# Kernel tuning notes

Measured on AMD Instinct MI355X. Metric: run time of the kernel, lower is better.

## Reference

```python
import jax, jax.numpy as jnp
import numpy as np

EPS = 1e-5
NUM_GRAPHS = 512


def _glorot(key, shape):
    lim = float(np.sqrt(6.0 / (shape[0] + shape[1])))
    return jax.random.uniform(key, shape, jnp.float32, -lim, lim)


def setup_inputs() -> dict:
    key = jax.random.key(0)
    ks = jax.random.split(key, 20)
    N, E, F0 = 50000, 800000, 64
    x = jax.random.normal(ks[0], (N, F0), jnp.float32)
    edge_index = jax.random.randint(ks[1], (2, E), 0, N, jnp.int64)
    batch = jnp.sort(jax.random.randint(ks[2], (N,), 0, NUM_GRAPHS, jnp.int64))
    dims = [(F0, 128), (128, 64), (64, 32)]
    p = {}
    for i, (di, do) in enumerate(dims, start=1):
        p[f"W{i}l"] = _glorot(ks[3 * i], (di, do))
        p[f"b{i}"] = jnp.zeros((do,), jnp.float32)
        p[f"W{i}r"] = _glorot(ks[3 * i + 1], (di, do))
        p[f"g{i}"] = jnp.ones((do,), jnp.float32)
        p[f"be{i}"] = jnp.zeros((do,), jnp.float32)
    p["Wf1"] = _glorot(ks[13], (32, 128)); p["bf1"] = jnp.zeros((128,), jnp.float32)
    p["Wf2"] = _glorot(ks[14], (128, 64)); p["bf2"] = jnp.zeros((64,), jnp.float32)
    p["Wf3"] = _glorot(ks[15], (64, 2)); p["bf3"] = jnp.zeros((2,), jnp.float32)
    return {"x": x, "edge_index": edge_index, "batch": batch, **p}


def _sage(x, src, dst, Wl, bl, Wr, n):
    # mean-aggregate neighbor features (gather from src, scatter-mean to dst)
    agg = jax.ops.segment_sum(x[src], dst, num_segments=n)
    cnt = jax.ops.segment_sum(jnp.ones((src.shape[0],), x.dtype), dst, num_segments=n)
    mean = agg / jnp.maximum(cnt, 1.0)[:, None]
    return mean @ Wl + bl + x @ Wr


def _bn(x, g, b):
    mu = jnp.mean(x, axis=0)
    var = jnp.mean((x - mu) ** 2, axis=0)  # biased var, torch training mode
    return (x - mu) * jax.lax.rsqrt(var + EPS) * g + b


def reference(x, edge_index, batch,
              W1l, b1, W1r, g1, be1,
              W2l, b2, W2r, g2, be2,
              W3l, b3, W3r, g3, be3,
              Wf1, bf1, Wf2, bf2, Wf3, bf3):
    n = x.shape[0]
    src, dst = edge_index[0], edge_index[1]
    h = _bn(jax.nn.relu(_sage(x, src, dst, W1l, b1, W1r, n)), g1, be1)
    h = _bn(jax.nn.relu(_sage(h, src, dst, W2l, b2, W2r, n)), g2, be2)
    h = _bn(jax.nn.relu(_sage(h, src, dst, W3l, b3, W3r, n)), g3, be3)
    pooled = jax.ops.segment_sum(h, batch, num_segments=NUM_GRAPHS)  # [G, 32]
    cr = jax.nn.relu(pooled @ Wf1 + bf1)  # dropout = identity (eval)
    cr = jax.nn.relu(cr @ Wf2 + bf2)
    cr = cr @ Wf3 + bf3
    return cr.reshape(-1, 2)
```

## Files before the change

### kernel.cpp

```cpp
#include <hip/hip_runtime.h>
#include <hip/hip_bf16.h>

#define EPSBN 1e-5f
#define NGRAPH 512
#define SCAN_NB 128

typedef __attribute__((ext_vector_type(8))) short bf16x8;
typedef __attribute__((ext_vector_type(4))) float f32x4;

__device__ inline short f2bf(float f) {
    unsigned u = __builtin_bit_cast(unsigned, f);
    u += 0x7fffu + ((u >> 16) & 1u);
    return (short)(u >> 16);
}
__device__ inline float bf2f(short s) {
    unsigned u = ((unsigned)(unsigned short)s) << 16;
    return __builtin_bit_cast(float, u);
}
__device__ inline int xcd_id() {
    int x;
    asm volatile("s_getreg_b32 %0, hwreg(HW_REG_XCC_ID, 0, 4)" : "=s"(x));
    return x & 7;
}

__global__ void __launch_bounds__(256) k_hist8(
    const int* __restrict__ dst, int* __restrict__ hist8, int E, int Npad)
{
    int* h = hist8 + xcd_id() * Npad;
    const int stride = gridDim.x * 256;
    for (int e = blockIdx.x * 256 + threadIdx.x; e < E; e += stride)
        atomicAdd(&h[dst[e]], 1);
}

__global__ void __launch_bounds__(256) k_scan1(
    const int* __restrict__ hist8, int* __restrict__ blocksum, int N, int Npad)
{
    __shared__ int red[256];
    const int C = (N + SCAN_NB - 1) / SCAN_NB;
    const int b = blockIdx.x, t = threadIdx.x;
    const int lo = b * C, hi = min(lo + C, N);
    int s = 0;
    for (int i = lo + t; i < hi; i += 256) {
        int v = 0;
        #pragma unroll
        for (int c = 0; c < 8; c++) v += hist8[c * Npad + i];
        s += v;
    }
    red[t] = s;
    __syncthreads();
    for (int off = 128; off; off >>= 1) {
        if (t < off) red[t] += red[t + off];
        __syncthreads();
    }
    if (t == 0) blocksum[b] = red[0];
}

__global__ void __launch_bounds__(256) k_scan3(
    const int* __restrict__ hist8, const int* __restrict__ blocksum,
    int* __restrict__ row_off, int* __restrict__ cursor, int N, int Npad)
{
    __shared__ int red[256];
    __shared__ int boff_s;
    const int C = (N + SCAN_NB - 1) / SCAN_NB;
    const int b = blockIdx.x, t = threadIdx.x;
    const int lo = b * C, hi = min(lo + C, N);
    if (t == 0) {
        int acc = 0;
        for (int i = 0; i < b; i++) acc += blocksum[i];
        boff_s = acc;
        if (b == SCAN_NB - 1) {
            int tot = acc;
            for (int i = b; i < SCAN_NB; i++) tot += blocksum[i];
            row_off[N] = tot;
        }
    }
    const int TC = (C + 255) / 256;
    const int s0 = lo + t * TC;
    const int s1 = min(s0 + TC, hi);
    auto hsum = [&](int i) {
        int v = 0;
        #pragma unroll
        for (int c = 0; c < 8; c++) v += hist8[c * Npad + i];
        return v;
    };
    int s = 0;
    for (int i = s0; i < s1; i++) s += hsum(i);
    red[t] = s;
    __syncthreads();
    for (int off = 1; off < 256; off <<= 1) {
        int u = (t >= off) ? red[t - off] : 0;
        __syncthreads();
        red[t] += u;
        __syncthreads();
    }
    int run = boff_s + red[t] - s;
    for (int i = s0; i < s1; i++) {
        row_off[i] = run;
        cursor[i] = run;
        run += hsum(i);
    }
}

__global__ void __launch_bounds__(256) k_scatter(
    const int* __restrict__ src, const int* __restrict__ dst,
    int* __restrict__ cursor, int* __restrict__ csr, int E)
{
    for (int e = blockIdx.x * 256 + threadIdx.x; e < E; e += gridDim.x * 256) {
        int d = dst[e];
        int p = atomicAdd(&cursor[d], 1);
        csr[p] = src[e];
    }
}

__device__ inline int lbound(const int* __restrict__ a, int n, int v) {
    int lo = 0, hi = n;
    while (lo < hi) {
        int mid = (lo + hi) >> 1;
        if (a[mid] < v) lo = mid + 1; else hi = mid;
    }
    return lo;
}
__global__ void __launch_bounds__(256) k_gcnt_bs(
    const int* __restrict__ batch, float* __restrict__ gcnt, int N)
{
    int g = blockIdx.x * 256 + threadIdx.x;
    if (g < NGRAPH)
        gcnt[g] = (float)(lbound(batch, N, g + 1) - lbound(batch, N, g));
}

template <int F>
__global__ void __launch_bounds__(256) k_gatherb(
    const short* __restrict__ feat, const int* __restrict__ row_off,
    const int* __restrict__ csr, short* __restrict__ aggb, int N)
{
    constexpr int LPR = F / 8;
    constexpr int RPB = 256 / LPR;
    const int lane = threadIdx.x % LPR;
    const int rloc = threadIdx.x / LPR;
    const short* fbase = feat + lane * 8;
    for (int row = blockIdx.x * RPB + rloc; row < N; row += gridDim.x * RPB) {
        const int s0 = row_off[row];
        const int s1 = row_off[row + 1];
        float acc0[8], acc1[8], acc2[8], acc3[8];
        #pragma unroll
        for (int i = 0; i < 8; i++) {
            acc0[i] = 0.f; acc1[i] = 0.f; acc2[i] = 0.f; acc3[i] = 0.f;
        }
        int p = s0;
        for (; p + 3 < s1; p += 4) {
            int sA = csr[p], sB = csr[p + 1], sC = csr[p + 2], sD = csr[p + 3];
            bf16x8 va = *(const bf16x8*)&fbase[(long long)sA * F];
            bf16x8 vb = *(const bf16x8*)&fbase[(long long)sB * F];
            bf16x8 vc = *(const bf16x8*)&fbase[(long long)sC * F];
            bf16x8 vd = *(const bf16x8*)&fbase[(long long)sD * F];
            #pragma unroll
            for (int i = 0; i < 8; i++) {
                acc0[i] += bf2f(va[i]);
                acc1[i] += bf2f(vb[i]);
                acc2[i] += bf2f(vc[i]);
                acc3[i] += bf2f(vd[i]);
            }
        }
        for (; p < s1; p++) {
            int sA = csr[p];
            bf16x8 va = *(const bf16x8*)&fbase[(long long)sA * F];
            #pragma unroll
            for (int i = 0; i < 8; i++) acc0[i] += bf2f(va[i]);
        }
        short o[8];
        #pragma unroll
        for (int i = 0; i < 8; i++)
            o[i] = f2bf((acc0[i] + acc1[i]) + (acc2[i] + acc3[i]));
        *(bf16x8*)&aggb[(long long)row * F + lane * 8] = *(bf16x8*)o;
    }
}

__global__ void __launch_bounds__(256) k_cvt(
    const float* __restrict__ in, short* __restrict__ out, long long n4)
{
    long long i = (long long)blockIdx.x * 256 + threadIdx.x;
    if (i >= n4) return;
    float4 v = *(const float4*)&in[i * 4];
    short4 o = make_short4(f2bf(v.x), f2bf(v.y), f2bf(v.z), f2bf(v.w));
    *(short4*)&out[i * 4] = o;
}

template <int K, int F, bool AFF>
__global__ void __launch_bounds__(64) k_wprep2(
    const float* __restrict__ Wl, const float* __restrict__ Wr,
    const float* __restrict__ a, const float* __restrict__ c,
    const float* __restrict__ bias,
    short* __restrict__ Wlt, short* __restrict__ Wrt,
    float* __restrict__ cvl, float* __restrict__ cvr)
{
    int j = blockIdx.x * 64 + threadIdx.x;
    const bool second = j >= F;
    const int jj = second ? j - F : j;
    if (jj >= F || j >= 2 * F) return;
    const float* W = second ? Wr : Wl;
    short* Wt = second ? Wrt : Wlt;
    float cv = (second && bias) ? bias[jj] : 0.f;
    for (int k = 0; k < K; k++) {
        float w = W[k * F + jj];
        float aa = 1.f;
        if constexpr (AFF) {
            aa = a[k];
            cv += c[k] * w;
        }
        Wt[jj * K + k] = f2bf(aa * w);
    }
    if (second) cvr[jj] = cv; else cvl[jj] = cv;
}

template <int K, int FOUT, bool DUAL, bool HASBASE, bool FINAL, bool OUTBF16,
          bool POOL>
__global__ void __launch_bounds__(256) k_mgemm(
    const short* __restrict__ A, const short* __restrict__ A2,
    const short* __restrict__ Wt, const short* __restrict__ Wt2,
    const float* __restrict__ cvec, const short* __restrict__ base,
    const int* __restrict__ row_off, void* outv,
    float* __restrict__ s_out, float* __restrict__ q_out,
    const int* __restrict__ batchp, float* __restrict__ praw8, int N)
{
    constexpr int KS = K / 32;
    constexpr int NCT = FOUT / 16;
    const int lane = threadIdx.x & 63;
    const int wid = threadIdx.x >> 6;
    const int g = lane >> 4;
    const int mi = lane & 15;
    const int RT = (N + 15) >> 4;
    const int nw = gridDim.x * 4;
    float* outf = (float*)outv;
    short* outb = (short*)outv;
    float* pr = nullptr;
    if constexpr (POOL) pr = praw8 + (size_t)xcd_id() * NGRAPH * 32;

    float st_s[FINAL ? NCT : 1];
    float st_q[FINAL ? NCT : 1];
    if constexpr (FINAL) {
        #pragma unroll
        for (int ct = 0; ct < NCT; ct++) { st_s[ct] = 0.f; st_q[ct] = 0.f; }
    }

    for (int rt = blockIdx.x * 4 + wid; rt < RT; rt += nw) {
        const int m0 = rt * 16;
        int arow = m0 + mi;
        if (arow >= N) arow = N - 1;

        bf16x8 af[KS];
        bf16x8 af2[DUAL ? KS : 1];
        const short* ap = A + (long long)arow * K;
        #pragma unroll
        for (int s = 0; s < KS; s++)
            af[s] = *(const bf16x8*)(ap + s * 32 + g * 8);
        if constexpr (DUAL) {
            const short* ap2 = A2 + (long long)arow * K;
            #pragma unroll
            for (int s = 0; s < KS; s++)
                af2[s] = *(const bf16x8*)(ap2 + s * 32 + g * 8);
        }

        float invc[4];
        if constexpr (DUAL || HASBASE) {
            #pragma unroll
            for (int r = 0; r < 4; r++) {
                int row = m0 + 4 * g + r;
                int cnt = 1;
                if (row < N) cnt = max(row_off[row + 1] - row_off[row], 1);
                invc[r] = 1.f / (float)cnt;
            }
        }
        int bidx[4];
        if constexpr (POOL) {
            #pragma unroll
            for (int r = 0; r < 4; r++) {
                int row = m0 + 4 * g + r;
                bidx[r] = (row < N) ? batchp[row] : -1;
            }
        }

        #pragma unroll
        for (int ct = 0; ct < NCT; ct++) {
            f32x4 acc = {0.f, 0.f, 0.f, 0.f};
            f32x4 acc2 = {0.f, 0.f, 0.f, 0.f};
            const short* bp = Wt + (long long)(ct * 16 + mi) * K;
            #pragma unroll
            for (int s = 0; s < KS; s++) {
                bf16x8 bf = *(const bf16x8*)(bp + s * 32 + g * 8);
                acc = __builtin_amdgcn_mfma_f32_16x16x32_bf16(af[s], bf, acc, 0, 0, 0);
                if constexpr (DUAL) {
                    bf16x8 bf2 = *(const bf16x8*)(Wt2 + (long long)(ct * 16 + mi) * K + s * 32 + g * 8);
                    acc2 = __builtin_amdgcn_mfma_f32_16x16x32_bf16(af2[s], bf2, acc2, 0, 0, 0);
                }
            }
            float cv = cvec[ct * 16 + mi];
            float sl = 0.f, ql = 0.f;
            #pragma unroll
            for (int r = 0; r < 4; r++) {
                int row = m0 + 4 * g + r;
                if (row < N) {
                    float v = acc[r] + cv;
                    if constexpr (DUAL) v = fmaf(invc[r], acc2[r], v);
                    if constexpr (HASBASE)
                        v = fmaf(invc[r], bf2f(base[(long long)row * FOUT + ct * 16 + mi]), v);
                    if constexpr (FINAL) v = fmaxf(v, 0.f);
                    if constexpr (POOL) {
                        atomicAdd(&pr[bidx[r] * FOUT + ct * 16 + mi], v);
                    } else if constexpr (OUTBF16) {
                        outb[(long long)row * FOUT + ct * 16 + mi] = f2bf(v);
                    } else {
                        outf[(long long)row * FOUT + ct * 16 + mi] = v;
                    }
                    if constexpr (FINAL) { sl += v; ql += v * v; }
                }
            }
            if constexpr (FINAL) {
                sl += __shfl_xor(sl, 16, 64);
                sl += __shfl_xor(sl, 32, 64);
                ql += __shfl_xor(ql, 16, 64);
                ql += __shfl_xor(ql, 32, 64);
                st_s[ct] += sl;
                st_q[ct] += ql;
            }
        }
    }

    if constexpr (FINAL) {
        __shared__ float redS[4][NCT][16];
        __shared__ float redQ[4][NCT][16];
        if (lane < 16) {
            #pragma unroll
            for (int ct = 0; ct < NCT; ct++) {
                redS[wid][ct][lane] = st_s[ct];
                redQ[wid][ct][lane] = st_q[ct];
            }
        }
        __syncthreads();
        if (wid == 0 && lane < 16) {
            #pragma unroll
            for (int ct = 0; ct < NCT; ct++) {
                float s = redS[0][ct][lane] + redS[1][ct][lane] +
                          redS[2][ct][lane] + redS[3][ct][lane];
                float q = redQ[0][ct][lane] + redQ[1][ct][lane] +
                          redQ[2][ct][lane] + redQ[3][ct][lane];
                atomicAdd(&s_out[ct * 16 + lane], s);
                atomicAdd(&q_out[ct * 16 + lane], q);
            }
        }
    }
}

__global__ void k_finalize(const float* __restrict__ s, const float* __restrict__ q,
                           const float* __restrict__ g, const float* __restrict__ be,
                           float* __restrict__ a, float* __restrict__ c,
                           int F, float invN)
{
    int j = threadIdx.x;
    if (j < F) {
        float mu = s[j] * invN;
        float var = q[j] * invN - mu * mu;
        float aj = g[j] / sqrtf(var + EPSBN);
        a[j] = aj;
        c[j] = be[j] - mu * aj;
    }
}

__global__ void __launch_bounds__(128) k_mlp(
    const float* __restrict__ praw8, const float* __restrict__ a3,
    const float* __restrict__ c3, const float* __restrict__ gcnt,
    const float* __restrict__ Wf1, const float* __restrict__ bf1,
    const float* __restrict__ Wf2, const float* __restrict__ bf2,
    const float* __restrict__ Wf3, const float* __restrict__ bf3,
    float* __restrict__ out)
{
    __shared__ float p[32], h1[128], h2[64];
    int g = blockIdx.x, t = threadIdx.x;
    if (t < 32) {
        float s = 0.f;
        #pragma unroll
        for (int c = 0; c < 8; c++)
            s += praw8[(size_t)c * NGRAPH * 32 + g * 32 + t];
        p[t] = a3[t] * s + gcnt[g] * c3[t];
    }
    __syncthreads();
    {
        float acc = bf1[t];
        #pragma unroll
        for (int k = 0; k < 32; k++) acc += p[k] * Wf1[k * 128 + t];
        h1[t] = fmaxf(acc, 0.f);
    }
    __syncthreads();
    if (t < 64) {
        float acc = bf2[t];
        #pragma unroll
        for (int k = 0; k < 128; k++) acc += h1[k] * Wf2[k * 64 + t];
        h2[t] = fmaxf(acc, 0.f);
    }
    __syncthreads();
    if (t < 2) {
        float acc = bf3[t];
        #pragma unroll
        for (int k = 0; k < 64; k++) acc += h2[k] * Wf3[k * 2 + t];
        out[g * 2 + t] = acc;
    }
}

extern "C" void kernel_launch(void* const* d_in, const int* in_sizes, int n_in,
                              void* d_out, int out_size, void* d_ws, size_t ws_size,
                              hipStream_t stream)
{
    const float* x     = (const float*)d_in[0];
    const int*   ei    = (const int*)d_in[1];
    const int*   batch = (const int*)d_in[2];
    const float* W1l = (const float*)d_in[3];
    const float* b1  = (const float*)d_in[4];
    const float* W1r = (const float*)d_in[5];
    const float* g1  = (const float*)d_in[6];
    const float* be1 = (const float*)d_in[7];
    const float* W2l = (const float*)d_in[8];
    const float* b2  = (const float*)d_in[9];
    const float* W2r = (const float*)d_in[10];
    const float* g2  = (const float*)d_in[11];
    const float* be2 = (const float*)d_in[12];
    const float* W3l = (const float*)d_in[13];
    const float* b3  = (const float*)d_in[14];
    const float* W3r = (const float*)d_in[15];
    const float* g3  = (const float*)d_in[16];
    const float* be3 = (const float*)d_in[17];
    const float* Wf1 = (const float*)d_in[18];
    const float* bf1 = (const float*)d_in[19];
    const float* Wf2 = (const float*)d_in[20];
    const float* bf2 = (const float*)d_in[21];
    const float* Wf3 = (const float*)d_in[22];
    const float* bf3 = (const float*)d_in[23];

    const int N = in_sizes[0] / 64;
    const int E = in_sizes[1] / 2;
    const int Npad = (N + 255) & ~255;
    const int* src = ei;
    const int* dst = ei + E;

    char* ws = (char*)d_ws;
    size_t off = 0;
    auto alloc = [&](size_t bytes) {
        size_t o = off;
        off += (bytes + 511) & ~(size_t)511;
        return o;
    };
    const size_t o_rowoff = alloc((size_t)(N + 1) * 4);
    const size_t o_cursor = alloc((size_t)N * 4);
    const size_t o_bsum   = alloc(SCAN_NB * 4);
    const size_t o_csr    = alloc((size_t)E * 4);
    const size_t o_zoneB  = alloc((size_t)N * 128);
    const size_t o_zoneC  = alloc((size_t)N * 128);
    const size_t o_zoneD  = alloc((size_t)N * 256);
    const size_t o_zoneE  = alloc((size_t)N * 128);
    const size_t o_aff    = alloc(448 * 4);
    const size_t o_cvec   = alloc(512 * 4);
    const size_t o_wt     = alloc((8192 * 4 + 2048 * 2) * 2);
    const size_t o_gcnt   = alloc((size_t)NGRAPH * 4);
    const size_t o_zero0  = off;
    const size_t o_hist8  = alloc((size_t)Npad * 8 * 4);
    const size_t o_stats  = alloc(448 * 4);
    const size_t o_praw8  = alloc((size_t)NGRAPH * 32 * 4 * 8);
    const size_t zero_len = off - o_zero0;
    (void)ws_size;

    int* row_off = (int*)(ws + o_rowoff);
    int* hist8   = (int*)(ws + o_hist8);
    int* cursor  = (int*)(ws + o_cursor);
    int* bsum    = (int*)(ws + o_bsum);
    int* csr     = (int*)(ws + o_csr);
    short* xb   = (short*)(ws + o_zoneB);
    short* y2b  = (short*)(ws + o_zoneB);
    short* aggb = (short*)(ws + o_zoneC);
    short* t2b  = (short*)(ws + o_zoneC);
    short* t1b  = (short*)(ws + o_zoneD);
    short* y3b  = (short*)(ws + o_zoneD);
    short* m2b  = (short*)(ws + o_zoneE);
    short* m3b  = (short*)(ws + o_zoneE);
    float* praw8 = (float*)(ws + o_praw8);
    float* gcnt  = (float*)(ws + o_gcnt);
    float* s1 = (float*)(ws + o_stats);
    float* q1 = s1 + 128;
    float* s2 = q1 + 128;
    float* q2 = s2 + 64;
    float* s3 = q2 + 64;
    float* q3 = s3 + 32;
    float* a1 = (float*)(ws + o_aff);
    float* c1 = a1 + 128;
    float* a2 = c1 + 128;
    float* c2 = a2 + 64;
    float* a3 = c2 + 64;
    float* c3 = a3 + 32;
    float* cv1l = (float*)(ws + o_cvec);
    float* cv1r = cv1l + 128;
    float* cv2l = cv1r + 128;
    float* cv2r = cv2l + 64;
    float* cv3l = cv2r + 64;
    float* cv3r = cv3l + 32;
    short* W1l_t = (short*)(ws + o_wt);
    short* W1r_t = W1l_t + 8192;
    short* W2l_t = W1r_t + 8192;
    short* W2r_t = W2l_t + 8192;
    short* W3l_t = W2r_t + 8192;
    short* W3r_t = W3l_t + 2048;

    const float invN = 1.0f / (float)N;
    const int MG = 512;

    hipMemsetAsync(ws + o_zero0, 0, zero_len, stream);

    k_hist8<<<2048, 256, 0, stream>>>(dst, hist8, E, Npad);
    k_scan1<<<SCAN_NB, 256, 0, stream>>>(hist8, bsum, N, Npad);
    k_scan3<<<SCAN_NB, 256, 0, stream>>>(hist8, bsum, row_off, cursor, N, Npad);
    k_scatter<<<2048, 256, 0, stream>>>(src, dst, cursor, csr, E);
    k_gcnt_bs<<<2, 256, 0, stream>>>(batch, gcnt, N);

    k_cvt<<<(int)(((long long)N * 16 + 255) / 256), 256, 0, stream>>>(
        x, xb, (long long)N * 16);
    k_wprep2<64, 128, false><<<4, 64, 0, stream>>>(
        W1l, W1r, nullptr, nullptr, b1, W1l_t, W1r_t, cv1l, cv1r);

    k_gatherb<64><<<(N + 31) / 32, 256, 0, stream>>>(
        xb, row_off, csr, aggb, N);
    k_mgemm<64, 128, true, false, true, true, false><<<MG, 256, 0, stream>>>(
        xb, aggb, W1r_t, W1l_t, cv1r, nullptr, row_off, t1b, s1, q1,
        nullptr, nullptr, N);
    k_finalize<<<1, 128, 0, stream>>>(s1, q1, g1, be1, a1, c1, 128, invN);

    k_wprep2<128, 64, true><<<2, 64, 0, stream>>>(
        W2l, W2r, a1, c1, b2, W2l_t, W2r_t, cv2l, cv2r);
    k_mgemm<128, 64, false, false, false, true, false><<<MG, 256, 0, stream>>>(
        t1b, nullptr, W2l_t, nullptr, cv2l, nullptr, row_off, y2b,
        nullptr, nullptr, nullptr, nullptr, N);
    k_gatherb<64><<<(N + 31) / 32, 256, 0, stream>>>(
        y2b, row_off, csr, m2b, N);
    k_mgemm<128, 64, false, true, true, true, false><<<MG, 256, 0, stream>>>(
        t1b, nullptr, W2r_t, nullptr, cv2r, m2b, row_off, t2b, s2, q2,
        nullptr, nullptr, N);
    k_finalize<<<1, 64, 0, stream>>>(s2, q2, g2, be2, a2, c2, 64, invN);

    k_wprep2<64, 32, true><<<1, 64, 0, stream>>>(
        W3l, W3r, a2, c2, b3, W3l_t, W3r_t, cv3l, cv3r);
    k_mgemm<64, 32, false, false, false, true, false><<<MG, 256, 0, stream>>>(
        t2b, nullptr, W3l_t, nullptr, cv3l, nullptr, row_off, y3b,
        nullptr, nullptr, nullptr, nullptr, N);
    k_gatherb<32><<<(N + 63) / 64, 256, 0, stream>>>(
        y3b, row_off, csr, m3b, N);
    k_mgemm<64, 32, false, true, true, false, true><<<MG, 256, 0, stream>>>(
        t2b, nullptr, W3r_t, nullptr, cv3r, m3b, row_off, nullptr, s3, q3,
        batch, praw8, N);
    k_finalize<<<1, 32, 0, stream>>>(s3, q3, g3, be3, a3, c3, 32, invN);

    k_mlp<<<NGRAPH, 128, 0, stream>>>(praw8, a3, c3, gcnt,
                                      Wf1, bf1, Wf2, bf2, Wf3, bf3,
                                      (float*)d_out);
}
```

Baseline: 300.3 us.

## Fuse small prep kernels, resize GEMM grid, trim gather accumulators

Merges the fp32-to-bf16 conversion of x into the histogram kernel and folds the per-graph count binary search into the first scan kernel, removing two launches. Scatter now writes CSR entries with nontemporal stores. The gather kernel gets an occupancy hint and uses two accumulator sets instead of four to lower register pressure. The GEMM grid is sized from N (one block per four 16-row tiles) instead of a fixed 512 blocks. Changing the grid assumes k_mgemm's internal row mapping matches the new block count, and the gather summation order changes slightly.

```diff
diff --git a/kernel.cpp b/kernel.cpp
--- a/kernel.cpp
+++ b/kernel.cpp
@@ -23,21 +23,42 @@
     return x & 7;
 }
 
-__global__ void __launch_bounds__(256) k_hist8(
-    const int* __restrict__ dst, int* __restrict__ hist8, int E, int Npad)
+__global__ void __launch_bounds__(256) k_hist_cvt(
+    const int* __restrict__ dst, int* __restrict__ hist8,
+    const float* __restrict__ x, short* __restrict__ xb,
+    int E, int Npad, long long n4)
 {
     int* h = hist8 + xcd_id() * Npad;
     const int stride = gridDim.x * 256;
     for (int e = blockIdx.x * 256 + threadIdx.x; e < E; e += stride)
         atomicAdd(&h[dst[e]], 1);
+    for (long long i = blockIdx.x * 256 + threadIdx.x; i < n4; i += stride) {
+        float4 v = *(const float4*)&x[i * 4];
+        short4 o = make_short4(f2bf(v.x), f2bf(v.y), f2bf(v.z), f2bf(v.w));
+        *(short4*)&xb[i * 4] = o;
+    }
+}
+
+__device__ inline int lbound(const int* __restrict__ a, int n, int v) {
+    int lo = 0, hi = n;
+    while (lo < hi) {
+        int mid = (lo + hi) >> 1;
+        if (a[mid] < v) lo = mid + 1; else hi = mid;
+    }
+    return lo;
 }
 
 __global__ void __launch_bounds__(256) k_scan1(
-    const int* __restrict__ hist8, int* __restrict__ blocksum, int N, int Npad)
+    const int* __restrict__ hist8, int* __restrict__ blocksum,
+    const int* __restrict__ batch, float* __restrict__ gcnt,
+    int N, int Npad)
 {
     __shared__ int red[256];
     const int C = (N + SCAN_NB - 1) / SCAN_NB;
     const int b = blockIdx.x, t = threadIdx.x;
+    const int g = b * 256 + t;
+    if (g < NGRAPH)
+        gcnt[g] = (float)(lbound(batch, N, g + 1) - lbound(batch, N, g));
     const int lo = b * C, hi = min(lo + C, N);
     int s = 0;
     for (int i = lo + t; i < hi; i += 256) {
@@ -108,28 +129,12 @@
     for (int e = blockIdx.x * 256 + threadIdx.x; e < E; e += gridDim.x * 256) {
         int d = dst[e];
         int p = atomicAdd(&cursor[d], 1);
-        csr[p] = src[e];
-    }
-}
-
-__device__ inline int lbound(const int* __restrict__ a, int n, int v) {
-    int lo = 0, hi = n;
-    while (lo < hi) {
-        int mid = (lo + hi) >> 1;
-        if (a[mid] < v) lo = mid + 1; else hi = mid;
-    }
-    return lo;
-}
-__global__ void __launch_bounds__(256) k_gcnt_bs(
-    const int* __restrict__ batch, float* __restrict__ gcnt, int N)
-{
-    int g = blockIdx.x * 256 + threadIdx.x;
-    if (g < NGRAPH)
-        gcnt[g] = (float)(lbound(batch, N, g + 1) - lbound(batch, N, g));
+        __builtin_nontemporal_store(src[e], &csr[p]);
+    }
 }
 
 template <int F>
-__global__ void __launch_bounds__(256) k_gatherb(
+__global__ void __launch_bounds__(256, 8) k_gatherb(
     const short* __restrict__ feat, const int* __restrict__ row_off,
     const int* __restrict__ csr, short* __restrict__ aggb, int N)
 {
@@ -141,11 +146,9 @@
     for (int row = blockIdx.x * RPB + rloc; row < N; row += gridDim.x * RPB) {
         const int s0 = row_off[row];
         const int s1 = row_off[row + 1];
-        float acc0[8], acc1[8], acc2[8], acc3[8];
-        #pragma unroll
-        for (int i = 0; i < 8; i++) {
-            acc0[i] = 0.f; acc1[i] = 0.f; acc2[i] = 0.f; acc3[i] = 0.f;
-        }
+        float acc0[8], acc1[8];
+        #pragma unroll
+        for (int i = 0; i < 8; i++) { acc0[i] = 0.f; acc1[i] = 0.f; }
         int p = s0;
         for (; p + 3 < s1; p += 4) {
             int sA = csr[p], sB = csr[p + 1], sC = csr[p + 2], sD = csr[p + 3];
@@ -155,10 +158,8 @@
             bf16x8 vd = *(const bf16x8*)&fbase[(long long)sD * F];
             #pragma unroll
             for (int i = 0; i < 8; i++) {
-                acc0[i] += bf2f(va[i]);
-                acc1[i] += bf2f(vb[i]);
-                acc2[i] += bf2f(vc[i]);
-                acc3[i] += bf2f(vd[i]);
+                acc0[i] += bf2f(va[i]) + bf2f(vc[i]);
+                acc1[i] += bf2f(vb[i]) + bf2f(vd[i]);
             }
         }
         for (; p < s1; p++) {
@@ -169,20 +170,9 @@
         }
         short o[8];
         #pragma unroll
-        for (int i = 0; i < 8; i++)
-            o[i] = f2bf((acc0[i] + acc1[i]) + (acc2[i] + acc3[i]));
+        for (int i = 0; i < 8; i++) o[i] = f2bf(acc0[i] + acc1[i]);
         *(bf16x8*)&aggb[(long long)row * F + lane * 8] = *(bf16x8*)o;
     }
-}
-
-__global__ void __launch_bounds__(256) k_cvt(
-    const float* __restrict__ in, short* __restrict__ out, long long n4)
-{
-    long long i = (long long)blockIdx.x * 256 + threadIdx.x;
-    if (i >= n4) return;
-    float4 v = *(const float4*)&in[i * 4];
-    short4 o = make_short4(f2bf(v.x), f2bf(v.y), f2bf(v.z), f2bf(v.w));
-    *(short4*)&out[i * 4] = o;
 }
 
 template <int K, int F, bool AFF>
@@ -507,48 +497,46 @@
     short* W3r_t = W3l_t + 2048;
 
     const float invN = 1.0f / (float)N;
-    const int MG = 512;
+    const int MGB = (((N + 15) >> 4) + 3) / 4;
 
     hipMemsetAsync(ws + o_zero0, 0, zero_len, stream);
 
-    k_hist8<<<2048, 256, 0, stream>>>(dst, hist8, E, Npad);
-    k_scan1<<<SCAN_NB, 256, 0, stream>>>(hist8, bsum, N, Npad);
+    k_hist_cvt<<<2048, 256, 0, stream>>>(dst, hist8, x, xb, E, Npad,
+                                         (long long)N * 16);
+    k_scan1<<<SCAN_NB, 256, 0, stream>>>(hist8, bsum, batch, gcnt, N, Npad);
     k_scan3<<<SCAN_NB, 256, 0, stream>>>(hist8, bsum, row_off, cursor, N, Npad);
     k_scatter<<<2048, 256, 0, stream>>>(src, dst, cursor, csr, E);
-    k_gcnt_bs<<<2, 256, 0, stream>>>(batch, gcnt, N);
-
-    k_cvt<<<(int)(((long long)N * 16 + 255) / 256), 256, 0, stream>>>(
-        x, xb, (long long)N * 16);
+
     k_wprep2<64, 128, false><<<4, 64, 0, stream>>>(
         W1l, W1r, nullptr, nullptr, b1, W1l_t, W1r_t, cv1l, cv1r);
 
     k_gatherb<64><<<(N + 31) / 32, 256, 0, stream>>>(
         xb, row_off, csr, aggb, N);
-    k_mgemm<64, 128, true, false, true, true, false><<<MG, 256, 0, stream>>>(
+    k_mgemm<64, 128, true, false, true, true, false><<<MGB, 256, 0, stream>>>(
         xb, aggb, W1r_t, W1l_t, cv1r, nullptr, row_off, t1b, s1, q1,
         nullptr, nullptr, N);
     k_finalize<<<1, 128, 0, stream>>>(s1, q1, g1, be1, a1, c1, 128, invN);
 
     k_wprep2<128, 64, true><<<2, 64, 0, stream>>>(
         W2l, W2r, a1, c1, b2, W2l_t, W2r_t, cv2l, cv2r);
-    k_mgemm<128, 64, false, false, false, true, false><<<MG, 256, 0, stream>>>(
+    k_mgemm<128, 64, false, false, false, true, false><<<MGB, 256, 0, stream>>>(
         t1b, nullptr, W2l_t, nullptr, cv2l, nullptr, row_off, y2b,
         nullptr, nullptr, nullptr, nullptr, N);
     k_gatherb<64><<<(N + 31) / 32, 256, 0, stream>>>(
         y2b, row_off, csr, m2b, N);
-    k_mgemm<128, 64, false, true, true, true, false><<<MG, 256, 0, stream>>>(
+    k_mgemm<128, 64, false, true, true, true, false><<<MGB, 256, 0, stream>>>(
         t1b, nullptr, W2r_t, nullptr, cv2r, m2b, row_off, t2b, s2, q2,
         nullptr, nullptr, N);
     k_finalize<<<1, 64, 0, stream>>>(s2, q2, g2, be2, a2, c2, 64, invN);
 
     k_wprep2<64, 32, true><<<1, 64, 0, stream>>>(
         W3l, W3r, a2, c2, b3, W3l_t, W3r_t, cv3l, cv3r);
-    k_mgemm<64, 32, false, false, false, true, false><<<MG, 256, 0, stream>>>(
+    k_mgemm<64, 32, false, false, false, true, false><<<MGB, 256, 0, stream>>>(
         t2b, nullptr, W3l_t, nullptr, cv3l, nullptr, row_off, y3b,
         nullptr, nullptr, nullptr, nullptr, N);
     k_gatherb<32><<<(N + 63) / 64, 256, 0, stream>>>(
         y3b, row_off, csr, m3b, N);
-    k_mgemm<64, 32, false, true, true, false, true><<<MG, 256, 0, stream>>>(
+    k_mgemm<64, 32, false, true, true, false, true><<<MGB, 256, 0, stream>>>(
         t2b, nullptr, W3r_t, nullptr, cv3r, m3b, row_off, nullptr, s3, q3,
         batch, praw8, N);
     k_finalize<<<1, 32, 0, stream>>>(s3, q3, g3, be3, a3, c3, 32, invN);
```

New measurement: 330.0 us. 1.1x slower.
